# Optimization experiments

Measured on AMD Instinct MI355X. Metric: run time of the kernel, lower is better.

## Reference

```python
import jax, jax.numpy as jnp
import numpy as np

D_MODEL, HID, N_NODES, NODE_DIM = 128, 256, 17, 32

def _gelu(x):
    return jax.nn.gelu(x, approximate=False)  # torch nn.GELU default (erf)

def setup_inputs() -> dict:
    key = jax.random.key(0)
    ks = jax.random.split(key, 12)
    B, W = 16, 4096
    x = jax.random.normal(ks[0], (B, W, D_MODEL), dtype=jnp.float32)
    # node_proj: Linear(128,256) -> GELU -> Linear(256, 17*32)
    W1 = jax.random.normal(ks[1], (D_MODEL, HID), dtype=jnp.float32) / np.sqrt(D_MODEL)
    b1 = jnp.zeros((HID,), jnp.float32)
    W2 = jax.random.normal(ks[2], (HID, N_NODES * NODE_DIM), dtype=jnp.float32) / np.sqrt(HID)
    b2 = jnp.zeros((N_NODES * NODE_DIM,), jnp.float32)
    # GAT1
    adj1 = jnp.eye(N_NODES, dtype=jnp.float32) * 5.0 + jax.random.normal(ks[3], (N_NODES, N_NODES), jnp.float32) * 0.05
    Wg1 = jax.random.normal(ks[4], (NODE_DIM, NODE_DIM), dtype=jnp.float32) / np.sqrt(NODE_DIM)
    bg1 = jnp.zeros((NODE_DIM,), jnp.float32)
    # GAT2
    adj2 = jnp.eye(N_NODES, dtype=jnp.float32) * 5.0 + jax.random.normal(ks[5], (N_NODES, N_NODES), jnp.float32) * 0.05
    Wg2 = jax.random.normal(ks[6], (NODE_DIM, NODE_DIM), dtype=jnp.float32) / np.sqrt(NODE_DIM)
    bg2 = jnp.zeros((NODE_DIM,), jnp.float32)
    # coord_proj: Linear(32, 2)
    Wc = jax.random.normal(ks[7], (NODE_DIM, 2), dtype=jnp.float32) / np.sqrt(NODE_DIM)
    bc = jnp.zeros((2,), jnp.float32)
    return {"x": x, "W1": W1, "b1": b1, "W2": W2, "b2": b2,
            "adj1": adj1, "Wg1": Wg1, "bg1": bg1,
            "adj2": adj2, "Wg2": Wg2, "bg2": bg2,
            "Wc": Wc, "bc": bc}

def _gat(nodes, adj_logits, Wg, bg):
    # nodes: [B, W, N, F]
    adj = jax.nn.softmax(adj_logits, axis=-1)          # [N, N]
    mixed = jnp.einsum('ij,bwjf->bwif', adj, nodes)    # graph conv over 17 joints
    return _gelu(mixed @ Wg + bg) + nodes              # linear-GELU + residual

def reference(x, W1, b1, W2, b2, adj1, Wg1, bg1, adj2, Wg2, bg2, Wc, bc):
    B, W, _ = x.shape
    h = _gelu(x @ W1 + b1)                 # [B, W, 256] (dropout inactive at eval)
    nodes = (h @ W2 + b2).reshape(B, W, N_NODES, NODE_DIM)
    out = _gat(nodes, adj1, Wg1, bg1)
    out = _gat(out, adj2, Wg2, bg2)
    return out @ Wc + bc                   # [B, W, 17, 2]
```

## Files before the change

kernel.cpp:

```cpp
#include <hip/hip_runtime.h>
#include <hip/hip_bf16.h>

using bf16 = __hip_bfloat16;
typedef __bf16 bf16x4v __attribute__((ext_vector_type(4)));
typedef __bf16 bf16x8 __attribute__((ext_vector_type(8)));
typedef float f32x4 __attribute__((ext_vector_type(4)));

#define MT 32
#define SX 136
#define SH 264
#define SJ 20
#define TFS 640
#define NTF_ELEMS 20480
#define MS_BASE 20496
#define SMS 36
#define MSW 1440
#define S_ELEMS 32304

__device__ __forceinline__ float bf2f(bf16 v) { return __bfloat162float(v); }

__device__ __forceinline__ float gelu_f(float x) {
    float u  = 0.7978845608f * x * (1.0f + 0.044715f * x * x);
    float au = fabsf(u);
    float e  = __expf(-2.0f * au);
    float t  = (1.0f - e) / (1.0f + e);
    t = (u < 0.0f) ? -t : t;
    return 0.5f * x * (1.0f + t);
}

__device__ __forceinline__ bf16x8 ld8(const bf16* p) {
    return *reinterpret_cast<const bf16x8*>(p);
}
__device__ __forceinline__ bf16x8 ld8u(const bf16* p) {
    bf16x4v lo = *reinterpret_cast<const bf16x4v*>(p);
    bf16x4v hi = *reinterpret_cast<const bf16x4v*>(p + 4);
    return __builtin_shufflevector(lo, hi, 0, 1, 2, 3, 4, 5, 6, 7);
}
__device__ __forceinline__ f32x4 mfma16(bf16x8 a, bf16x8 b, f32x4 c) {
    return __builtin_amdgcn_mfma_f32_16x16x32_bf16(a, b, c, 0, 0, 0);
}

__global__ void prep_kernel(const float* __restrict__ W1, const float* __restrict__ W2,
                            const float* __restrict__ Wg1, const float* __restrict__ Wg2,
                            const float* __restrict__ adj1, const float* __restrict__ adj2,
                            bf16* __restrict__ w1t, bf16* __restrict__ w2t,
                            bf16* __restrict__ wg1t, bf16* __restrict__ wg2t,
                            float* __restrict__ A1f, float* __restrict__ A2f) {
    int idx = blockIdx.x * 256 + threadIdx.x;
    if (idx < 32768) {
        int r = idx >> 8, c = idx & 255;
        w1t[c * 128 + r] = __float2bfloat16(W1[idx]);
    } else if (idx < 172032) {
        int j = idx - 32768;
        int r = j / 544, c = j % 544;
        w2t[c * 256 + r] = __float2bfloat16(W2[j]);
    } else if (idx < 173056) {
        int j = idx - 172032;
        wg1t[(j & 31) * 32 + (j >> 5)] = __float2bfloat16(Wg1[j]);
    } else if (idx < 174080) {
        int j = idx - 173056;
        wg2t[(j & 31) * 32 + (j >> 5)] = __float2bfloat16(Wg2[j]);
    }
    if (blockIdx.x == 0) {
        int t = threadIdx.x;
        if (t < 17 || (t >= 32 && t < 49)) {
            const float* adj = (t < 17) ? adj1 : adj2;
            float*       A   = (t < 17) ? A1f  : A2f;
            int row = (t < 17) ? t : (t - 32);
            float v[17]; float mx = -1e30f;
            for (int j = 0; j < 17; ++j) { v[j] = adj[row * 17 + j]; mx = fmaxf(mx, v[j]); }
            float s = 0.0f;
            for (int j = 0; j < 17; ++j) { v[j] = __expf(v[j] - mx); s += v[j]; }
            float inv = 1.0f / s;
            for (int j = 0; j < 17; ++j) A[row * 17 + j] = v[j] * inv;
        }
    }
}

__global__ __launch_bounds__(512, 4)
void gat_main(const float* __restrict__ x,
              const float* __restrict__ b1, const float* __restrict__ b2,
              const float* __restrict__ bg1, const float* __restrict__ bg2,
              const bf16* __restrict__ w1t, const bf16* __restrict__ w2t,
              const bf16* __restrict__ wg1t, const bf16* __restrict__ wg2t,
              const float* __restrict__ A1, const float* __restrict__ A2,
              const float* __restrict__ Wc, const float* __restrict__ bc,
              float* __restrict__ out) {
    __shared__ alignas(16) bf16 S[S_ELEMS];
    bf16* xs = S;
    bf16* hs = S + 4352;

    const int tid  = threadIdx.x;
    const int w    = tid >> 6;
    const int lane = tid & 63;
    const int l    = lane & 15;
    const int q    = lane >> 4;
    const int t0   = blockIdx.x * MT;

    for (int c = tid; c < 1024; c += 512) {
        int row = c >> 5, c4 = c & 31;
        const float4 v = *reinterpret_cast<const float4*>(x + (size_t)(t0 + row) * 128 + c4 * 4);
        bf16 tmp[4] = { __float2bfloat16(v.x), __float2bfloat16(v.y),
                        __float2bfloat16(v.z), __float2bfloat16(v.w) };
        *reinterpret_cast<ushort4*>(xs + row * SX + c4 * 4) =
            *reinterpret_cast<const ushort4*>(tmp);
    }
    __syncthreads();

    for (int nt = w * 2; nt < w * 2 + 2; ++nt) {
        int n = nt * 16 + l;
        bf16x8 bfr[4];
        const bf16* wp = w1t + n * 128 + q * 8;
#pragma unroll
        for (int kf = 0; kf < 4; ++kf) bfr[kf] = ld8(wp + kf * 32);
        float bias = b1[n];
#pragma unroll
        for (int mt = 0; mt < 2; ++mt) {
            f32x4 acc = {0.f, 0.f, 0.f, 0.f};
            const bf16* ap = xs + (mt * 16 + l) * SX + q * 8;
#pragma unroll
            for (int kf = 0; kf < 4; ++kf)
                acc = mfma16(ld8(ap + kf * 32), bfr[kf], acc);
            int trow = mt * 16 + q * 4;
#pragma unroll
            for (int r = 0; r < 4; ++r)
                hs[(trow + r) * SH + n] = __float2bfloat16(gelu_f(acc[r] + bias));
        }
    }
    __syncthreads();

    {
        bf16x8 af[2][8];
#pragma unroll
        for (int mt = 0; mt < 2; ++mt)
#pragma unroll
            for (int kf = 0; kf < 8; ++kf)
                af[mt][kf] = ld8(hs + (mt * 16 + l) * SH + kf * 32 + q * 8);
        __syncthreads();

        for (int z = tid; z < 3072; z += 512) {
            int row = z / 3, k = z - row * 3;
            S[row * SJ + 17 + k] = __float2bfloat16(0.f);
        }
        if (tid < 16) S[NTF_ELEMS + tid] = __float2bfloat16(0.f);

        for (int nt = w; nt < 34; nt += 8) {
            int n = nt * 16 + l;
            float bias = b2[n];
            int i = n >> 5, f = n & 31;
            f32x4 a0 = {0.f, 0.f, 0.f, 0.f}, a1 = {0.f, 0.f, 0.f, 0.f};
            const bf16* wp = w2t + n * 256 + q * 8;
#pragma unroll
            for (int kf = 0; kf < 8; ++kf) {
                bf16x8 bfr = ld8(wp + kf * 32);
                a0 = mfma16(af[0][kf], bfr, a0);
                a1 = mfma16(af[1][kf], bfr, a1);
            }
#pragma unroll
            for (int mt = 0; mt < 2; ++mt) {
                const f32x4 acc = mt ? a1 : a0;
#pragma unroll
                for (int r = 0; r < 4; ++r) {
                    int t = mt * 16 + q * 4 + r;
                    S[t * TFS + f * SJ + i] = __float2bfloat16(acc[r] + bias);
                }
            }
        }
    }
    __syncthreads();

    bf16* ms_w = S + MS_BASE + w * MSW;

    for (int g = 0; g < 2; ++g) {
        const float* A  = g ? A2 : A1;
        const bf16* wgt = g ? wg2t : wg1t;
        const float* bg = g ? bg2 : bg1;

        bf16x8 mixB[2];
#pragma unroll
        for (int nt = 0; nt < 2; ++nt) {
            int i = nt * 16 + l;
            bf16 tmp[8];
#pragma unroll
            for (int e = 0; e < 8; ++e) {
                int j = q * 8 + e;
                float v = (i < 17 && j < 17) ? A[i * 17 + j] : 0.0f;
                tmp[e] = __float2bfloat16(v);
            }
            mixB[nt] = *reinterpret_cast<bf16x8*>(tmp);
        }
        bf16x8 wfr[2];
#pragma unroll
        for (int nt = 0; nt < 2; ++nt) wfr[nt] = ld8(wgt + (nt * 16 + l) * 32 + q * 8);
        float bgf[2] = { bg[l], bg[16 + l] };

        for (int c = 0; c < 2; ++c) {
#pragma unroll
            for (int mt2 = 0; mt2 < 4; ++mt2) {
                int R = w * 128 + c * 64 + mt2 * 16 + l;
                bf16x8 afr = ld8u(S + R * SJ + q * 8);
                int rr0 = mt2 * 16 + q * 4;
                int f0  = rr0 & 31;
                int tl  = rr0 >> 5;
#pragma unroll
                for (int nt = 0; nt < 2; ++nt) {
                    f32x4 acc = {0.f, 0.f, 0.f, 0.f};
                    acc = mfma16(afr, mixB[nt], acc);
                    int i = nt * 16 + l;
                    if (i < 17) {
                        union { ushort4 u; bf16 b[4]; } pk;
#pragma unroll
                        for (int r = 0; r < 4; ++r) pk.b[r] = __float2bfloat16(acc[r]);
                        *reinterpret_cast<ushort4*>(ms_w + (i * 2 + tl) * SMS + f0) = pk.u;
                    }
                }
            }

#pragma unroll
            for (int mt = 0; mt < 3; ++mt) {
                bf16x8 afr = ld8u(ms_w + (mt * 16 + l) * SMS + q * 8);
#pragma unroll
                for (int nt = 0; nt < 2; ++nt) {
                    f32x4 acc = {0.f, 0.f, 0.f, 0.f};
                    acc = mfma16(afr, wfr[nt], acc);
                    int fp = nt * 16 + l;
#pragma unroll
                    for (int r = 0; r < 4; ++r) {
                        int rr = mt * 16 + q * 4 + r;
                        int i  = rr >> 1;
                        int tl = rr & 1;
                        if (i < 17) {
                            int off = (w * 4 + c * 2 + tl) * TFS + fp * SJ + i;
                            float v = gelu_f(acc[r] + bgf[nt]) + bf2f(S[off]);
                            S[off]  = __float2bfloat16(v);
                        }
                    }
                }
            }
        }
    }

    for (int s = lane; s < 68; s += 64) {
        int tl = s / 17, i = s - tl * 17;
        int t  = w * 4 + tl;
        const bf16* gp = S + t * TFS + i;
        float o0 = bc[0], o1 = bc[1];
#pragma unroll
        for (int f = 0; f < 32; ++f) {
            float v = bf2f(gp[f * SJ]);
            o0 = fmaf(v, Wc[f * 2 + 0], o0);
            o1 = fmaf(v, Wc[f * 2 + 1], o1);
        }
        float2 pr = { o0, o1 };
        reinterpret_cast<float2*>(out)[(size_t)(t0 + t) * 17 + i] = pr;
    }
}

extern "C" void kernel_launch(void* const* d_in, const int* in_sizes, int n_in,
                              void* d_out, int out_size, void* d_ws, size_t ws_size,
                              hipStream_t stream) {
    const float* x    = (const float*)d_in[0];
    const float* W1   = (const float*)d_in[1];
    const float* b1   = (const float*)d_in[2];
    const float* W2   = (const float*)d_in[3];
    const float* b2   = (const float*)d_in[4];
    const float* adj1 = (const float*)d_in[5];
    const float* Wg1  = (const float*)d_in[6];
    const float* bg1  = (const float*)d_in[7];
    const float* adj2 = (const float*)d_in[8];
    const float* Wg2  = (const float*)d_in[9];
    const float* bg2  = (const float*)d_in[10];
    const float* Wc   = (const float*)d_in[11];
    const float* bc   = (const float*)d_in[12];

    char* ws = (char*)d_ws;
    bf16*  w1t  = (bf16*)(ws + 0);
    bf16*  w2t  = (bf16*)(ws + 65536);
    bf16*  wg1t = (bf16*)(ws + 344064);
    bf16*  wg2t = (bf16*)(ws + 346112);
    float* A1f  = (float*)(ws + 348160);
    float* A2f  = (float*)(ws + 349376);

    prep_kernel<<<680, 256, 0, stream>>>(W1, W2, Wg1, Wg2, adj1, adj2,
                                         w1t, w2t, wg1t, wg2t, A1f, A2f);

    const int tokens = 16 * 4096;
    gat_main<<<tokens / MT, 512, 0, stream>>>(x, b1, b2, bg1, bg2,
                                              w1t, w2t, wg1t, wg2t,
                                              A1f, A2f, Wc, bc, (float*)d_out);
}
```

Baseline: 249.8 us.

## Restructure GAT stage per timestep, shrink LDS, vectorize residual and output projection

The GAT inner loop now processes one timestep per iteration instead of two interleaved, which shrinks the per-warp mixing scratch and total shared memory, and the launch bounds ask for 6 blocks per CU instead of 4. The residual GELU update reads and writes 4 packed bf16 values at once instead of scalar accesses. The final coordinate projection spreads the feature reduction across lanes with shuffle reductions instead of looping serially over features per lane. GELU is rewritten with FMAs and a hardware reciprocal, which adds slight rounding differences and may raise register pressure under the tighter launch bound.

```diff
diff --git a/kernel.cpp b/kernel.cpp
--- a/kernel.cpp
+++ b/kernel.cpp
@@ -14,18 +14,19 @@
 #define NTF_ELEMS 20480
 #define MS_BASE 20496
 #define SMS 36
-#define MSW 1440
-#define S_ELEMS 32304
+#define MSW 612
+#define S_ELEMS 25936
 
 __device__ __forceinline__ float bf2f(bf16 v) { return __bfloat162float(v); }
 
 __device__ __forceinline__ float gelu_f(float x) {
-    float u  = 0.7978845608f * x * (1.0f + 0.044715f * x * x);
+    float u  = x * fmaf(0.035677408f * x, x, 0.7978845608f);
     float au = fabsf(u);
     float e  = __expf(-2.0f * au);
-    float t  = (1.0f - e) / (1.0f + e);
+    float t  = (1.0f - e) * __builtin_amdgcn_rcpf(1.0f + e);
     t = (u < 0.0f) ? -t : t;
-    return 0.5f * x * (1.0f + t);
+    float hx = 0.5f * x;
+    return fmaf(hx, t, hx);
 }
 
 __device__ __forceinline__ bf16x8 ld8(const bf16* p) {
@@ -77,7 +78,7 @@
     }
 }
 
-__global__ __launch_bounds__(512, 4)
+__global__ __launch_bounds__(512, 6)
 void gat_main(const float* __restrict__ x,
               const float* __restrict__ b1, const float* __restrict__ b2,
               const float* __restrict__ bg1, const float* __restrict__ bg2,
@@ -194,14 +195,14 @@
         for (int nt = 0; nt < 2; ++nt) wfr[nt] = ld8(wgt + (nt * 16 + l) * 32 + q * 8);
         float bgf[2] = { bg[l], bg[16 + l] };
 
-        for (int c = 0; c < 2; ++c) {
-#pragma unroll
-            for (int mt2 = 0; mt2 < 4; ++mt2) {
-                int R = w * 128 + c * 64 + mt2 * 16 + l;
+        for (int c = 0; c < 4; ++c) {
+            const int T = w * 4 + c;
+
+#pragma unroll
+            for (int mt2 = 0; mt2 < 2; ++mt2) {
+                int R = T * 32 + mt2 * 16 + l;
                 bf16x8 afr = ld8u(S + R * SJ + q * 8);
-                int rr0 = mt2 * 16 + q * 4;
-                int f0  = rr0 & 31;
-                int tl  = rr0 >> 5;
+                int f0 = mt2 * 16 + q * 4;
 #pragma unroll
                 for (int nt = 0; nt < 2; ++nt) {
                     f32x4 acc = {0.f, 0.f, 0.f, 0.f};
@@ -211,48 +212,90 @@
                         union { ushort4 u; bf16 b[4]; } pk;
 #pragma unroll
                         for (int r = 0; r < 4; ++r) pk.b[r] = __float2bfloat16(acc[r]);
-                        *reinterpret_cast<ushort4*>(ms_w + (i * 2 + tl) * SMS + f0) = pk.u;
+                        *reinterpret_cast<ushort4*>(ms_w + i * SMS + f0) = pk.u;
                     }
                 }
             }
 
 #pragma unroll
-            for (int mt = 0; mt < 3; ++mt) {
+            for (int mt = 0; mt < 2; ++mt) {
                 bf16x8 afr = ld8u(ms_w + (mt * 16 + l) * SMS + q * 8);
+                int i0 = mt * 16 + q * 4;
 #pragma unroll
                 for (int nt = 0; nt < 2; ++nt) {
                     f32x4 acc = {0.f, 0.f, 0.f, 0.f};
                     acc = mfma16(afr, wfr[nt], acc);
                     int fp = nt * 16 + l;
-#pragma unroll
-                    for (int r = 0; r < 4; ++r) {
-                        int rr = mt * 16 + q * 4 + r;
-                        int i  = rr >> 1;
-                        int tl = rr & 1;
-                        if (i < 17) {
-                            int off = (w * 4 + c * 2 + tl) * TFS + fp * SJ + i;
-                            float v = gelu_f(acc[r] + bgf[nt]) + bf2f(S[off]);
-                            S[off]  = __float2bfloat16(v);
+                    if (i0 < 17) {
+                        bf16* p = S + T * TFS + fp * SJ + i0;
+                        union { ushort4 u; bf16 b[4]; } old, nw;
+                        old.u = *reinterpret_cast<const ushort4*>(p);
+#pragma unroll
+                        for (int r = 0; r < 4; ++r) {
+                            float v = gelu_f(acc[r] + bgf[nt]) + bf2f(old.b[r]);
+                            if (i0 + r > 16) v = 0.0f;
+                            nw.b[r] = __float2bfloat16(v);
                         }
+                        *reinterpret_cast<ushort4*>(p) = nw.u;
                     }
                 }
             }
         }
     }
 
-    for (int s = lane; s < 68; s += 64) {
-        int tl = s / 17, i = s - tl * 17;
-        int t  = w * 4 + tl;
-        const bf16* gp = S + t * TFS + i;
-        float o0 = bc[0], o1 = bc[1];
-#pragma unroll
-        for (int f = 0; f < 32; ++f) {
-            float v = bf2f(gp[f * SJ]);
-            o0 = fmaf(v, Wc[f * 2 + 0], o0);
-            o1 = fmaf(v, Wc[f * 2 + 1], o1);
-        }
-        float2 pr = { o0, o1 };
-        reinterpret_cast<float2*>(out)[(size_t)(t0 + t) * 17 + i] = pr;
+    {
+        const int tL  = lane >> 4;
+        const int sub = lane & 15;
+        const int T   = w * 4 + tL;
+        const int i0  = (sub >> 2) * 4;
+        const int f0  = (sub & 3) * 8;
+        const bf16* base = S + T * TFS + i0;
+        float oa[4] = {0.f, 0.f, 0.f, 0.f}, ob[4] = {0.f, 0.f, 0.f, 0.f};
+#pragma unroll
+        for (int fo = 0; fo < 8; ++fo) {
+            int f = f0 + fo;
+            union { ushort4 u; bf16 b[4]; } pk;
+            pk.u = *reinterpret_cast<const ushort4*>(base + f * SJ);
+            float wc0 = Wc[f * 2], wc1 = Wc[f * 2 + 1];
+#pragma unroll
+            for (int r = 0; r < 4; ++r) {
+                float v = bf2f(pk.b[r]);
+                oa[r] = fmaf(v, wc0, oa[r]);
+                ob[r] = fmaf(v, wc1, ob[r]);
+            }
+        }
+#pragma unroll
+        for (int d = 1; d <= 2; d <<= 1)
+#pragma unroll
+            for (int r = 0; r < 4; ++r) {
+                oa[r] += __shfl_xor(oa[r], d);
+                ob[r] += __shfl_xor(ob[r], d);
+            }
+        if ((sub & 3) == 0) {
+            float bc0 = bc[0], bc1 = bc[1];
+#pragma unroll
+            for (int r = 0; r < 4; ++r) {
+                float2 pr = { oa[r] + bc0, ob[r] + bc1 };
+                reinterpret_cast<float2*>(out)[(size_t)(t0 + T) * 17 + i0 + r] = pr;
+            }
+        }
+        if (sub < 4) {
+            const bf16* b16p = S + T * TFS + 16;
+            float o0 = 0.f, o1 = 0.f;
+#pragma unroll
+            for (int fo = 0; fo < 8; ++fo) {
+                int f = sub * 8 + fo;
+                float v = bf2f(b16p[f * SJ]);
+                o0 = fmaf(v, Wc[f * 2], o0);
+                o1 = fmaf(v, Wc[f * 2 + 1], o1);
+            }
+            o0 += __shfl_xor(o0, 1); o1 += __shfl_xor(o1, 1);
+            o0 += __shfl_xor(o0, 2); o1 += __shfl_xor(o1, 2);
+            if (sub == 0) {
+                float2 pr = { o0 + bc[0], o1 + bc[1] };
+                reinterpret_cast<float2*>(out)[(size_t)(t0 + T) * 17 + 16] = pr;
+            }
+        }
     }
 }
 
```

Result: slower. 261.0 us (+4.5%).
